# Kernel optimization log

Hardware: AMD Instinct MI355X
Metric: run time of the kernel (lower is better)

The kernel has to match this reference:

```python
import jax, jax.numpy as jnp
import numpy as np


def conv1x1(x, w, b):
    # x: (B,C,H,W), w: (O,C), b: (O,)
    return jnp.einsum('bchw,oc->bohw', x, w) + b[None, :, None, None]


def maxpool2x2(x):
    B, C, H, W = x.shape
    return x.reshape(B, C, H // 2, 2, W // 2, 2).max(axis=(3, 5))


def setup_inputs() -> dict:
    key = jax.random.key(0)
    ks = jax.random.split(key, 10)
    B, C, H, W = 16, 256, 64, 64
    K = 8
    ck, ch = C // K, C // 2  # 32, 128
    sc = lambda fan_in: 1.0 / np.sqrt(fan_in)
    return {
        'x': jax.random.normal(ks[0], (B, C, H, W), jnp.float32),
        'wf': jax.random.normal(ks[1], (ck, C), jnp.float32) * sc(C),
        'bf': jnp.zeros((ck,), jnp.float32),
        'wg': jax.random.normal(ks[2], (ck, C), jnp.float32) * sc(C),
        'bg': jnp.zeros((ck,), jnp.float32),
        'wh': jax.random.normal(ks[3], (ch, C), jnp.float32) * sc(C),
        'bh': jnp.zeros((ch,), jnp.float32),
        'wv': jax.random.normal(ks[4], (C, ch), jnp.float32) * sc(ch),
        'bv': jnp.zeros((C,), jnp.float32),
        'gamma': jnp.float32(0.5),  # nonzero so the attention branch matters
    }


def reference(x, wf, bf, wg, bg, wh, bh, wv, bv, gamma):
    B, C, H, W = x.shape
    HW = H * W
    f = conv1x1(x, wf, bf).reshape(B, -1, HW)            # (B, C/K, HW)
    g = maxpool2x2(conv1x1(x, wg, bg))                    # (B, C/K, H/2, W/2)
    h = maxpool2x2(conv1x1(x, wh, bh))                    # (B, C/2, H/2, W/2)
    HWp = HW // 4
    g = g.reshape(B, -1, HWp)
    h = h.reshape(B, -1, HWp)
    s = jnp.einsum('bck,bcl->bkl', f, g)                  # (B, HW, HW')
    beta = jax.nn.softmax(s, axis=-1)
    o = jnp.einsum('bjk,blk->bjl', h, beta)               # (B, C/2, HW)
    o = o.reshape(B, -1, H, W)
    return gamma * conv1x1(o, wv, bv) + x
```

## Files before the change

### kernel.cpp

```cpp
#include <hip/hip_runtime.h>
#include <hip/hip_bf16.h>
#include <stdint.h>

#define B_N   16
#define C_N   256
#define W_N   64
#define HW_N  4096
#define CK_N  32
#define CH_N  128
#define HWP_N 1024
#define MR_N  192

typedef __attribute__((ext_vector_type(8))) short short8;
typedef __attribute__((ext_vector_type(4))) short short4v;
typedef __attribute__((ext_vector_type(4))) float f32x4;

#define MFMA(a, b, c) __builtin_amdgcn_mfma_f32_16x16x32_bf16((a), (b), (c), 0, 0, 0)

__device__ __forceinline__ f32x4 MFMA16B(short4v a, short4v b, f32x4 c) {
#if __has_builtin(__builtin_amdgcn_mfma_f32_16x16x16bf16_1k)
    return __builtin_amdgcn_mfma_f32_16x16x16bf16_1k(a, b, c, 0, 0, 0);
#else
    asm("v_mfma_f32_16x16x16_bf16 %0, %1, %2, %0" : "+v"(c) : "v"(a), "v"(b));
    return c;
#endif
}

__device__ __forceinline__ unsigned short f2bf(float f) {
    union { float f; unsigned u; } v; v.f = f;
    unsigned r = v.u + 0x7FFFu + ((v.u >> 16) & 1u);
    return (unsigned short)(r >> 16);
}
__device__ __forceinline__ unsigned packrn(float lo, float hi) {
    unsigned a = __float_as_uint(lo) + 0x8000u;
    unsigned b = __float_as_uint(hi) + 0x8000u;
    return __builtin_amdgcn_perm(b, a, 0x07060302);
}
__device__ __forceinline__ short8 ld8(const void* p) {
    return *reinterpret_cast<const short8*>(p);
}

__global__ __launch_bounds__(256) void k_prep(
    const float* __restrict__ wf, const float* __restrict__ wg,
    const float* __restrict__ wh, const float* __restrict__ wv,
    unsigned short* __restrict__ Wc, unsigned short* __restrict__ Wv)
{
    int i = blockIdx.x * 256 + threadIdx.x;
    if (i < MR_N * C_N) {
        int r = i / C_N, c = i % C_N;
        float v = (r < 32) ? wf[r * C_N + c]
                : (r < 64) ? wg[(r - 32) * C_N + c]
                           : wh[(r - 64) * C_N + c];
        Wc[i] = f2bf(v);
    }
    if (i < C_N * CH_N) Wv[i] = f2bf(wv[i]);
}

__global__ __launch_bounds__(256) void k_conv_fgh(
    const float* __restrict__ x, const unsigned short* __restrict__ Wc,
    const float* __restrict__ bfp, const float* __restrict__ bgp, const float* __restrict__ bhp,
    unsigned short* __restrict__ f_, unsigned short* __restrict__ g_, unsigned short* __restrict__ h_)
{
    __shared__ __align__(16) unsigned char lds[64 * 512];
    const int T = threadIdx.x;
    const int lane = T & 63, wid = T >> 6;
    const int blk = blockIdx.x;
    const int b = blk >> 6;
    const int seg = blk & 63;
    const int rp = seg >> 1;
    const int half = seg & 1;
    const float* xb = x + (size_t)b * C_N * HW_N;

    #pragma unroll
    for (int i = 0; i < 8; ++i) {
        int task = i * 256 + T;
        int pq = task & 15;
        int cp = task >> 4;
        int px0 = pq * 4;
        int row = 2 * rp + (px0 >> 5);
        int wcol = half * 32 + (px0 & 31);
        const float4 v0 = *reinterpret_cast<const float4*>(xb + (size_t)(2 * cp) * HW_N + row * W_N + wcol);
        const float4 v1 = *reinterpret_cast<const float4*>(xb + (size_t)(2 * cp + 1) * HW_N + row * W_N + wcol);
        float vlo[4] = {v0.x, v0.y, v0.z, v0.w};
        float vhi[4] = {v1.x, v1.y, v1.z, v1.w};
        int kc = cp >> 2, co = cp & 3;
        #pragma unroll
        for (int j = 0; j < 4; ++j) {
            int px = px0 + j;
            *reinterpret_cast<unsigned*>(lds + px * 512 + ((kc ^ (px & 31)) << 4) + co * 4)
                = packrn(vlo[j], vhi[j]);
        }
    }
    __syncthreads();

    const int l15 = lane & 15, quad = lane >> 4;
    f32x4 acc[3][4];
    #pragma unroll
    for (int mt = 0; mt < 3; ++mt)
        #pragma unroll
        for (int nt = 0; nt < 4; ++nt)
            acc[mt][nt] = f32x4{0.f, 0.f, 0.f, 0.f};

    const int m0base = wid * 48;
    for (int k0 = 0; k0 < 256; k0 += 32) {
        short8 afr[3];
        #pragma unroll
        for (int mt = 0; mt < 3; ++mt)
            afr[mt] = ld8(Wc + (size_t)(m0base + mt * 16 + l15) * C_N + k0 + quad * 8);
        #pragma unroll
        for (int nt = 0; nt < 4; ++nt) {
            int px = nt * 16 + l15;
            int kc = (k0 >> 3) + quad;
            short8 bfr = ld8(lds + px * 512 + ((kc ^ (px & 31)) << 4));
            #pragma unroll
            for (int mt = 0; mt < 3; ++mt)
                acc[mt][nt] = MFMA(afr[mt], bfr, acc[mt][nt]);
        }
    }

    #pragma unroll
    for (int mt = 0; mt < 3; ++mt) {
        int mbase = m0base + mt * 16;
        int mrow0 = mbase + quad * 4;
        float bias[4];
        #pragma unroll
        for (int r = 0; r < 4; ++r) {
            int m = mrow0 + r;
            bias[r] = (m < 32) ? bfp[m] : (m < 64) ? bgp[m - 32] : bhp[m - 64];
        }
        if (mbase < 32) {
            #pragma unroll
            for (int nt = 0; nt < 4; ++nt) {
                int px = nt * 16 + l15;
                int p = (2 * rp + (px >> 5)) * W_N + half * 32 + (px & 31);
                uint2 u;
                u.x = packrn(acc[mt][nt][0] + bias[0], acc[mt][nt][1] + bias[1]);
                u.y = packrn(acc[mt][nt][2] + bias[2], acc[mt][nt][3] + bias[3]);
                *reinterpret_cast<uint2*>(f_ + ((size_t)b * HW_N + p) * CK_N + mrow0) = u;
            }
        } else if (mbase < 64) {
            int gc0 = mrow0 - 32;
            #pragma unroll
            for (int nt = 0; nt < 2; ++nt) {
                float pv[4];
                #pragma unroll
                for (int r = 0; r < 4; ++r) {
                    float m1 = fmaxf(acc[mt][nt][r], acc[mt][nt + 2][r]);
                    pv[r] = fmaxf(m1, __shfl_xor(m1, 1)) + bias[r];
                }
                if ((lane & 1) == 0) {
                    int kp = rp * 32 + half * 16 + ((nt * 16 + l15) >> 1);
                    uint2 u;
                    u.x = packrn(pv[0], pv[1]);
                    u.y = packrn(pv[2], pv[3]);
                    *reinterpret_cast<uint2*>(g_ + ((size_t)b * HWP_N + kp) * CK_N + gc0) = u;
                }
            }
        } else {
            int hc0 = mrow0 - 64;
            #pragma unroll
            for (int nt = 0; nt < 2; ++nt) {
                float pv[4];
                #pragma unroll
                for (int r = 0; r < 4; ++r) {
                    float m1 = fmaxf(acc[mt][nt][r], acc[mt][nt + 2][r]);
                    pv[r] = fmaxf(m1, __shfl_xor(m1, 1)) + bias[r];
                }
                #pragma unroll
                for (int r = 0; r < 4; ++r) {
                    int lo = (int)(packrn(pv[r], pv[r]) & 0xFFFFu);
                    int hi = __shfl_down(lo, 2);
                    if ((lane & 3) == 0) {
                        int kp2 = rp * 32 + half * 16 + nt * 8 + (l15 >> 1);
                        *reinterpret_cast<unsigned*>(
                            h_ + ((size_t)b * CH_N + hc0 + r) * HWP_N + kp2)
                            = (unsigned)lo | ((unsigned)hi << 16);
                    }
                }
            }
        }
    }
}

__global__ __launch_bounds__(256, 4) void k_attn(
    const unsigned short* __restrict__ f_, const unsigned short* __restrict__ g_,
    const unsigned short* __restrict__ h_, unsigned short* __restrict__ o_)
{
    __shared__ __align__(16) unsigned char Vl[128 * 136];
    const int T = threadIdx.x;
    const int lane = T & 63, wid = T >> 6;
    const int l15 = lane & 15, quad = lane >> 4;

    const int blk = blockIdx.x;
    const int b = blk >> 6;
    const int q0w = (blk & 63) * 64 + wid * 16;
    const unsigned short* fb = f_ + (size_t)b * HW_N * CK_N;
    const unsigned short* gb = g_ + (size_t)b * HWP_N * CK_N;
    const unsigned short* hb = h_ + (size_t)b * CH_N * HWP_N;

    short8 ffr = ld8(fb + (size_t)(q0w + l15) * CK_N + quad * 8);

    const f32x4 zf = {0.f, 0.f, 0.f, 0.f};
    f32x4 oacc[8];
    #pragma unroll
    for (int ct = 0; ct < 8; ++ct)
        oacc[ct] = f32x4{0.f, 0.f, 0.f, 0.f};
    float lsum = 0.f;

    const int sch = T >> 3, skq = T & 7;
    uint4 vpre[4];
    #pragma unroll
    for (int i = 0; i < 4; ++i)
        vpre[i] = *reinterpret_cast<const uint4*>(hb + (size_t)(sch + i * 32) * HWP_N + skq * 8);
    short8 gcur[4];
    #pragma unroll
    for (int kt = 0; kt < 4; ++kt)
        gcur[kt] = ld8(gb + (size_t)(kt * 16 + l15) * CK_N + quad * 8);

    for (int c = 0; c < 16; ++c) {
        const int key0 = c * 64;
        __syncthreads();
        #pragma unroll
        for (int i = 0; i < 4; ++i) {
            unsigned char* dst = Vl + (sch + i * 32) * 136 + skq * 16;
            *reinterpret_cast<uint2*>(dst)     = uint2{vpre[i].x, vpre[i].y};
            *reinterpret_cast<uint2*>(dst + 8) = uint2{vpre[i].z, vpre[i].w};
        }
        if (c < 15) {
            #pragma unroll
            for (int i = 0; i < 4; ++i)
                vpre[i] = *reinterpret_cast<const uint4*>(
                    hb + (size_t)(sch + i * 32) * HWP_N + key0 + 64 + skq * 8);
        }
        __syncthreads();

        f32x4 sp[4];
        #pragma unroll
        for (int kt = 0; kt < 4; ++kt)
            sp[kt] = MFMA(gcur[kt], ffr, zf);
        if (c < 15) {
            #pragma unroll
            for (int kt = 0; kt < 4; ++kt)
                gcur[kt] = ld8(gb + (size_t)(key0 + 64 + kt * 16 + l15) * CK_N + quad * 8);
        }

        short4v pf[4];
        float lw = 0.f;
        #pragma unroll
        for (int kt = 0; kt < 4; ++kt) {
            float p0 = __builtin_amdgcn_exp2f(sp[kt][0] * 1.44269504f - 28.85390082f);
            float p1 = __builtin_amdgcn_exp2f(sp[kt][1] * 1.44269504f - 28.85390082f);
            float p2 = __builtin_amdgcn_exp2f(sp[kt][2] * 1.44269504f - 28.85390082f);
            float p3 = __builtin_amdgcn_exp2f(sp[kt][3] * 1.44269504f - 28.85390082f);
            lw += (p0 + p1) + (p2 + p3);
            uint2 u{packrn(p0, p1), packrn(p2, p3)};
            pf[kt] = __builtin_bit_cast(short4v, u);
        }
        lsum += lw;

        const int vbase = l15 * 136 + quad * 8;
        #pragma unroll
        for (int ct = 0; ct < 8; ++ct) {
            #pragma unroll
            for (int kt = 0; kt < 4; ++kt) {
                short4v afr = *reinterpret_cast<const short4v*>(Vl + vbase + ct * 2176 + kt * 32);
                oacc[ct] = MFMA16B(afr, pf[kt], oacc[ct]);
            }
        }
    }

    lsum += __shfl_xor(lsum, 16); lsum += __shfl_xor(lsum, 32);
    const float rl = 1.f / lsum;
    unsigned short* ob = o_ + (size_t)b * HW_N * CH_N;
    const int q = q0w + l15;
    #pragma unroll
    for (int ct = 0; ct < 8; ++ct) {
        uint2 u;
        u.x = packrn(oacc[ct][0] * rl, oacc[ct][1] * rl);
        u.y = packrn(oacc[ct][2] * rl, oacc[ct][3] * rl);
        *reinterpret_cast<uint2*>(ob + (size_t)q * CH_N + ct * 16 + quad * 4) = u;
    }
}

__global__ __launch_bounds__(256) void k_out(
    const unsigned short* __restrict__ o_, const unsigned short* __restrict__ Wv,
    const float* __restrict__ bv, const float* __restrict__ x,
    const float* __restrict__ gamma_p, float* __restrict__ out)
{
    __shared__ __align__(16) unsigned char lds[64 * 272];
    const int T = threadIdx.x;
    const int lane = T & 63, wid = T >> 6;
    const int blk = blockIdx.x;
    const int b = blk >> 6;
    const int p0 = (blk & 63) * 64;
    const unsigned short* ob = o_ + ((size_t)b * HW_N + p0) * CH_N;

    #pragma unroll
    for (int i = 0; i < 4; ++i) {
        int task = i * 256 + T;
        int p = task >> 4, kc = task & 15;
        short8 v = ld8(ob + p * CH_N + kc * 8);
        *reinterpret_cast<short8*>(lds + p * 272 + kc * 16) = v;
    }
    __syncthreads();

    const int l15 = lane & 15, quad = lane >> 4;
    f32x4 acc[4][4];
    #pragma unroll
    for (int mt = 0; mt < 4; ++mt)
        #pragma unroll
        for (int nt = 0; nt < 4; ++nt)
            acc[mt][nt] = f32x4{0.f, 0.f, 0.f, 0.f};

    const int m0b = wid * 64;
    #pragma unroll
    for (int k0 = 0; k0 < 128; k0 += 32) {
        short8 bfr[4];
        #pragma unroll
        for (int nt = 0; nt < 4; ++nt)
            bfr[nt] = ld8(lds + (nt * 16 + l15) * 272 + k0 * 2 + quad * 16);
        #pragma unroll
        for (int mt = 0; mt < 4; ++mt) {
            short8 afr = ld8(Wv + (size_t)(m0b + mt * 16 + l15) * CH_N + k0 + quad * 8);
            #pragma unroll
            for (int nt = 0; nt < 4; ++nt)
                acc[mt][nt] = MFMA(bfr[nt], afr, acc[mt][nt]);
        }
    }

    const float gamma = *gamma_p;
    const float* xb = x + (size_t)b * C_N * HW_N;
    float* outb = out + (size_t)b * C_N * HW_N;
    #pragma unroll
    for (int mt = 0; mt < 4; ++mt) {
        int oc = m0b + mt * 16 + l15;
        float bvv = bv[oc];
        #pragma unroll
        for (int nt = 0; nt < 4; ++nt) {
            size_t base = (size_t)oc * HW_N + p0 + nt * 16 + quad * 4;
            float4 xv = *reinterpret_cast<const float4*>(xb + base);
            float4 ov;
            ov.x = gamma * (acc[mt][nt][0] + bvv) + xv.x;
            ov.y = gamma * (acc[mt][nt][1] + bvv) + xv.y;
            ov.z = gamma * (acc[mt][nt][2] + bvv) + xv.z;
            ov.w = gamma * (acc[mt][nt][3] + bvv) + xv.w;
            *reinterpret_cast<float4*>(outb + base) = ov;
        }
    }
}

extern "C" void kernel_launch(void* const* d_in, const int* in_sizes, int n_in,
                              void* d_out, int out_size, void* d_ws, size_t ws_size,
                              hipStream_t stream) {
    const float* x     = (const float*)d_in[0];
    const float* wf    = (const float*)d_in[1];
    const float* bf    = (const float*)d_in[2];
    const float* wg    = (const float*)d_in[3];
    const float* bg    = (const float*)d_in[4];
    const float* wh    = (const float*)d_in[5];
    const float* bh    = (const float*)d_in[6];
    const float* wv    = (const float*)d_in[7];
    const float* bv    = (const float*)d_in[8];
    const float* gamma = (const float*)d_in[9];
    float* out = (float*)d_out;
    char* ws = (char*)d_ws;

    unsigned short* f_ = (unsigned short*)(ws);
    unsigned short* g_ = (unsigned short*)(ws + 4194304);
    unsigned short* h_ = (unsigned short*)(ws + 5242880);
    unsigned short* o_ = (unsigned short*)(ws + 9437184);
    unsigned short* Wc = (unsigned short*)(ws + 26214400);
    unsigned short* Wv = (unsigned short*)(ws + 26312704);

    k_prep<<<192, 256, 0, stream>>>(wf, wg, wh, wv, Wc, Wv);
    k_conv_fgh<<<1024, 256, 0, stream>>>(x, Wc, bf, bg, bh, f_, g_, h_);
    k_attn<<<1024, 256, 0, stream>>>(f_, g_, h_, o_);
    k_out<<<1024, 256, 0, stream>>>(o_, Wv, bv, x, gamma, out);
}
```

Baseline: 211.1 us.

## Double-buffer V tile in attention and drop LDS staging in output projection

The attention kernel now double-buffers the LDS V tile, which removes one of the two block barriers per key chunk. This lets the write of the next tile overlap with MFMA reads of the current one, at the cost of twice the LDS per block. The output-projection kernel drops its shared-memory staging and barrier. Each wave now independently computes a 64x64 output tile, loading o directly from global memory. That adds redundant global reads of o (four waves per pixel block) in exchange for no sync and higher occupancy.

```diff
diff --git a/kernel.cpp b/kernel.cpp
--- a/kernel.cpp
+++ b/kernel.cpp
@@ -186,7 +186,7 @@
     const unsigned short* __restrict__ f_, const unsigned short* __restrict__ g_,
     const unsigned short* __restrict__ h_, unsigned short* __restrict__ o_)
 {
-    __shared__ __align__(16) unsigned char Vl[128 * 136];
+    __shared__ __align__(16) unsigned char Vl[2 * 17408];
     const int T = threadIdx.x;
     const int lane = T & 63, wid = T >> 6;
     const int l15 = lane & 15, quad = lane >> 4;
@@ -218,11 +218,10 @@
         gcur[kt] = ld8(gb + (size_t)(kt * 16 + l15) * CK_N + quad * 8);
 
     for (int c = 0; c < 16; ++c) {
-        const int key0 = c * 64;
-        __syncthreads();
+        unsigned char* buf = Vl + (c & 1) * 17408;
         #pragma unroll
         for (int i = 0; i < 4; ++i) {
-            unsigned char* dst = Vl + (sch + i * 32) * 136 + skq * 16;
+            unsigned char* dst = buf + (sch + i * 32) * 136 + skq * 16;
             *reinterpret_cast<uint2*>(dst)     = uint2{vpre[i].x, vpre[i].y};
             *reinterpret_cast<uint2*>(dst + 8) = uint2{vpre[i].z, vpre[i].w};
         }
@@ -230,7 +229,7 @@
             #pragma unroll
             for (int i = 0; i < 4; ++i)
                 vpre[i] = *reinterpret_cast<const uint4*>(
-                    hb + (size_t)(sch + i * 32) * HWP_N + key0 + 64 + skq * 8);
+                    hb + (size_t)(sch + i * 32) * HWP_N + (c + 1) * 64 + skq * 8);
         }
         __syncthreads();
 
@@ -241,7 +240,7 @@
         if (c < 15) {
             #pragma unroll
             for (int kt = 0; kt < 4; ++kt)
-                gcur[kt] = ld8(gb + (size_t)(key0 + 64 + kt * 16 + l15) * CK_N + quad * 8);
+                gcur[kt] = ld8(gb + (size_t)((c + 1) * 64 + kt * 16 + l15) * CK_N + quad * 8);
         }
 
         short4v pf[4];
@@ -263,7 +262,7 @@
         for (int ct = 0; ct < 8; ++ct) {
             #pragma unroll
             for (int kt = 0; kt < 4; ++kt) {
-                short4v afr = *reinterpret_cast<const short4v*>(Vl + vbase + ct * 2176 + kt * 32);
+                short4v afr = *reinterpret_cast<const short4v*>(buf + vbase + ct * 2176 + kt * 32);
                 oacc[ct] = MFMA16B(afr, pf[kt], oacc[ct]);
             }
         }
@@ -282,29 +281,21 @@
     }
 }
 
-__global__ __launch_bounds__(256) void k_out(
+__global__ __launch_bounds__(256, 4) void k_out(
     const unsigned short* __restrict__ o_, const unsigned short* __restrict__ Wv,
     const float* __restrict__ bv, const float* __restrict__ x,
     const float* __restrict__ gamma_p, float* __restrict__ out)
 {
-    __shared__ __align__(16) unsigned char lds[64 * 272];
     const int T = threadIdx.x;
     const int lane = T & 63, wid = T >> 6;
-    const int blk = blockIdx.x;
-    const int b = blk >> 6;
-    const int p0 = (blk & 63) * 64;
-    const unsigned short* ob = o_ + ((size_t)b * HW_N + p0) * CH_N;
-
-    #pragma unroll
-    for (int i = 0; i < 4; ++i) {
-        int task = i * 256 + T;
-        int p = task >> 4, kc = task & 15;
-        short8 v = ld8(ob + p * CH_N + kc * 8);
-        *reinterpret_cast<short8*>(lds + p * 272 + kc * 16) = v;
-    }
-    __syncthreads();
-
     const int l15 = lane & 15, quad = lane >> 4;
+    const int w = blockIdx.x * 4 + wid;
+    const int b = w >> 8;
+    const int rem = w & 255;
+    const int oc0 = (rem >> 6) * 64;
+    const int px0 = (rem & 63) * 64;
+    const unsigned short* ob = o_ + ((size_t)b * HW_N + px0) * CH_N;
+
     f32x4 acc[4][4];
     #pragma unroll
     for (int mt = 0; mt < 4; ++mt)
@@ -312,16 +303,15 @@
         for (int nt = 0; nt < 4; ++nt)
             acc[mt][nt] = f32x4{0.f, 0.f, 0.f, 0.f};
 
-    const int m0b = wid * 64;
     #pragma unroll
     for (int k0 = 0; k0 < 128; k0 += 32) {
         short8 bfr[4];
         #pragma unroll
         for (int nt = 0; nt < 4; ++nt)
-            bfr[nt] = ld8(lds + (nt * 16 + l15) * 272 + k0 * 2 + quad * 16);
+            bfr[nt] = ld8(ob + (size_t)(nt * 16 + l15) * CH_N + k0 + quad * 8);
         #pragma unroll
         for (int mt = 0; mt < 4; ++mt) {
-            short8 afr = ld8(Wv + (size_t)(m0b + mt * 16 + l15) * CH_N + k0 + quad * 8);
+            short8 afr = ld8(Wv + (size_t)(oc0 + mt * 16 + l15) * CH_N + k0 + quad * 8);
             #pragma unroll
             for (int nt = 0; nt < 4; ++nt)
                 acc[mt][nt] = MFMA(bfr[nt], afr, acc[mt][nt]);
@@ -333,11 +323,11 @@
     float* outb = out + (size_t)b * C_N * HW_N;
     #pragma unroll
     for (int mt = 0; mt < 4; ++mt) {
-        int oc = m0b + mt * 16 + l15;
+        int oc = oc0 + mt * 16 + l15;
         float bvv = bv[oc];
         #pragma unroll
         for (int nt = 0; nt < 4; ++nt) {
-            size_t base = (size_t)oc * HW_N + p0 + nt * 16 + quad * 4;
+            size_t base = (size_t)oc * HW_N + px0 + nt * 16 + quad * 4;
             float4 xv = *reinterpret_cast<const float4*>(xb + base);
             float4 ov;
             ov.x = gamma * (acc[mt][nt][0] + bvv) + xv.x;
```

Measured after the change: 207.8 us. About the same (-1.6%).
